# Optimization experiments

Measured on AMD Instinct MI355X. Metric: run time of the kernel, lower is better.

The kernel has to match this reference:

```python
import jax, jax.numpy as jnp
import numpy as np

N, E = 50000, 800000
IN, HID, PROJ = 256, 256, 256


def setup_inputs() -> dict:
    key = jax.random.key(0)
    ks = jax.random.split(key, 6)
    x = jax.random.normal(ks[0], (N, IN), dtype=jnp.float32)
    edge_index = jax.random.randint(ks[1], (2, E), 0, N, dtype=jnp.int32)
    # GCNConv params: Linear (no bias inside lin; bias added after aggregation)
    W1 = jax.random.normal(ks[2], (IN, HID), dtype=jnp.float32) / np.sqrt(IN)
    b1 = jnp.zeros((HID,), dtype=jnp.float32)
    W2 = jax.random.normal(ks[3], (HID, PROJ), dtype=jnp.float32) / np.sqrt(HID)
    b2 = jnp.zeros((PROJ,), dtype=jnp.float32)
    # shared PReLU parameter (PyTorch default init 0.25, single shared scalar)
    a = jnp.asarray(0.25, dtype=jnp.float32)
    return {"x": x, "W1": W1, "b1": b1, "W2": W2, "b2": b2, "a": a,
            "edge_index": edge_index}


def _prelu(x, a):
    return jnp.where(x >= 0, x, a * x)


def _gcn_conv(x, W, b, src, dst, norm):
    # GCNConv: out = D^-1/2 (A + I) D^-1/2 (x W) + b
    h = x @ W                                      # [N, out]
    msg = h[src] * norm[:, None]                   # [E+N, out] edge messages
    out = jax.ops.segment_sum(msg, dst, num_segments=N)
    return out + b


def reference(x, W1, b1, W2, b2, a, edge_index):
    src, dst = edge_index[0], edge_index[1]
    loop = jnp.arange(N, dtype=src.dtype)
    src = jnp.concatenate([src, loop])             # add self-loops
    dst = jnp.concatenate([dst, loop])
    # symmetric normalization (degree counted on dst, as in PyG gcn_norm)
    deg = jax.ops.segment_sum(jnp.ones_like(dst, jnp.float32), dst,
                              num_segments=N)
    dinv = jax.lax.rsqrt(jnp.maximum(deg, 1.0))    # deg >= 1 with self-loops
    norm = dinv[src] * dinv[dst]                   # [E+N]
    h = _prelu(_gcn_conv(x, W1, b1, src, dst, norm), a)
    h = _prelu(_gcn_conv(h, W2, b2, src, dst, norm), a)
    return h
```

## Files before the change

### kernel.cpp

```cpp
#include <hip/hip_runtime.h>

#define NN 50000
#define EE 800000
#define FF 256
#define CAP 64
#define GEMM_BLKS 784
#define FILL_BLKS 3125

typedef float    f32x4 __attribute__((ext_vector_type(4)));
typedef _Float16 f16x8 __attribute__((ext_vector_type(8)));
typedef _Float16 f16x4 __attribute__((ext_vector_type(4)));

__global__ void packw_kernel(const float* __restrict__ W1, const float* __restrict__ W2,
                             _Float16* __restrict__ wp,
                             const int* __restrict__ ei, int* __restrict__ cnt,
                             int* __restrict__ ecw) {
    if (blockIdx.x >= 64) {
        int e = (blockIdx.x - 64) * 256 + threadIdx.x;
        int s = ei[e];
        int d = ei[EE + e];
        int slot = atomicAdd(&cnt[d], 1);
        if (slot < CAP) ecw[(size_t)d * CAP + slot] = s;
        return;
    }
    int idx = blockIdx.x * 256 + threadIdx.x;
    int p   = idx & 511;
    int kt  = (idx >> 9) & 7;
    int nb  = (idx >> 12) & 1;
    int L   = (idx >> 13) & 1;
    const float* W = L ? W2 : W1;
    int rs = p >> 2, cs = p & 3;
    int r  = rs ^ ((rs >> 2) & 1);
    int c  = cs ^ (r & 3);
    int n  = nb * 128 + r;
    int k0 = kt * 32 + c * 8;
    f16x8 hi, lo;
#pragma unroll
    for (int j = 0; j < 8; ++j) {
        float v = W[(size_t)(k0 + j) * 256 + n];
        _Float16 h = (_Float16)v;
        hi[j] = h;
        lo[j] = (_Float16)(v - (float)h);
    }
    size_t ch = ((size_t)((L * 2 + 0) * 2 + nb) * 8 + kt) * 4096;
    size_t cl = ((size_t)((L * 2 + 1) * 2 + nb) * 8 + kt) * 4096;
    *(f16x8*)(wp + ch + (size_t)p * 8) = hi;
    *(f16x8*)(wp + cl + (size_t)p * 8) = lo;
}


__device__ __forceinline__ void gll16(const void* g, void* l) {
    __builtin_amdgcn_global_load_lds(
        (const __attribute__((address_space(1))) void*)g,
        (__attribute__((address_space(3))) void*)l, 16, 0, 0);
}

template<typename AT>
__global__ __launch_bounds__(512) void gemm_kernel(
    const AT* __restrict__ X, const _Float16* __restrict__ Bhi,
    const _Float16* __restrict__ Blo, _Float16* __restrict__ H,
    const int* __restrict__ cnt) {
    __shared__ __align__(16) _Float16 Bh[2][4096];
    __shared__ __align__(16) _Float16 Bl[2][4096];
    __shared__ __align__(16) _Float16 As[2][4096];

    const int gid = blockIdx.x;
    const int p_  = (gid >> 4) * 8 + (gid & 7);
    const int nb  = (gid >> 3) & 1;
    if (p_ >= 391) return;

    const int tid = threadIdx.x;
    const int ln  = tid & 63;
    const int w   = tid >> 6;
    const int wm  = w & 1;
    const int wn  = w >> 1;
    const int q   = ln >> 4;
    const int l16 = ln & 15;
    const int m0  = p_ * 128;
    const size_t bchunk = (size_t)nb * 8 * 4096;

    const int g   = w * 64 + ln;
    const int rs_ = g >> 2, cs_ = g & 3;
    const int r_  = rs_ ^ ((rs_ >> 2) & 1);
    const int c_  = cs_ ^ (r_ & 3);
    int gm_ = m0 + r_; if (gm_ > NN - 1) gm_ = NN - 1;

    f32x4 acc[4][2] = {};

    auto stageB = [&](int kt, int buf) {
        gll16(Bhi + bchunk + (size_t)kt * 4096 + (size_t)g * 8,
              &Bh[buf][w * 512]);
        gll16(Blo + bchunk + (size_t)kt * 4096 + (size_t)g * 8,
              &Bl[buf][w * 512]);
    };
    auto stageA16 = [&](int kt, int buf) {
        gll16((const _Float16*)X + (size_t)gm_ * FF + kt * 32 + c_ * 8,
              (_Float16*)&As[buf][0] + (size_t)(w * 64) * 8);
    };
    auto loadA32 = [&](int kt, f32x4& v0, f32x4& v1) {
        const float* p = (const float*)X + (size_t)gm_ * FF + kt * 32 + c_ * 8;
        v0 = *(const f32x4*)p;
        v1 = *(const f32x4*)(p + 4);
    };
    auto writeA32 = [&](int buf, f32x4 v0, f32x4 v1) {
        f16x8 a;
        a[0] = (_Float16)v0.x; a[1] = (_Float16)v0.y;
        a[2] = (_Float16)v0.z; a[3] = (_Float16)v0.w;
        a[4] = (_Float16)v1.x; a[5] = (_Float16)v1.y;
        a[6] = (_Float16)v1.z; a[7] = (_Float16)v1.w;
        *(f16x8*)(&As[buf][(size_t)g * 8]) = a;
    };

    auto compute = [&](int buf) {
        f16x8 af[4], bhf[2], blf[2];
#pragma unroll
        for (int mt = 0; mt < 4; ++mt) {
            int r  = wm * 64 + mt * 16 + l16;
            int rr = r ^ ((r >> 2) & 1);
            af[mt] = *(const f16x8*)(&As[buf][(rr * 4 + (q ^ (r & 3))) * 8]);
        }
#pragma unroll
        for (int nt = 0; nt < 2; ++nt) {
            int r  = wn * 32 + nt * 16 + l16;
            int rr = r ^ ((r >> 2) & 1);
            int off = (rr * 4 + (q ^ (r & 3))) * 8;
            bhf[nt] = *(const f16x8*)(&Bh[buf][off]);
            blf[nt] = *(const f16x8*)(&Bl[buf][off]);
        }
#pragma unroll
        for (int mt = 0; mt < 4; ++mt)
#pragma unroll
            for (int nt = 0; nt < 2; ++nt) {
                acc[mt][nt] = __builtin_amdgcn_mfma_f32_16x16x32_f16(af[mt], bhf[nt], acc[mt][nt], 0, 0, 0);
                acc[mt][nt] = __builtin_amdgcn_mfma_f32_16x16x32_f16(af[mt], blf[nt], acc[mt][nt], 0, 0, 0);
            }
    };

    int cur = 0;
    if constexpr (sizeof(AT) == 4) {
        f32x4 v0, v1;
        loadA32(0, v0, v1);
        stageB(0, 0);
        writeA32(0, v0, v1);
        __syncthreads();
#pragma unroll
        for (int kt = 0; kt < 8; ++kt) {
            f32x4 n0, n1;
            if (kt < 7) {
                loadA32(kt + 1, n0, n1);
                stageB(kt + 1, cur ^ 1);
            }
            compute(cur);
            if (kt < 7) writeA32(cur ^ 1, n0, n1);
            __syncthreads();
            cur ^= 1;
        }
    } else {
        stageA16(0, 0);
        stageB(0, 0);
        __syncthreads();
#pragma unroll
        for (int kt = 0; kt < 8; ++kt) {
            if (kt < 7) { stageA16(kt + 1, cur ^ 1); stageB(kt + 1, cur ^ 1); }
            compute(cur);
            __syncthreads();
            cur ^= 1;
        }
    }

#pragma unroll
    for (int mt = 0; mt < 4; ++mt)
#pragma unroll
        for (int r4 = 0; r4 < 4; ++r4) {
            int m = m0 + wm * 64 + mt * 16 + q * 4 + r4;
            if (m < NN) {
                float sc = rsqrtf((float)(cnt[m] + 1));
#pragma unroll
                for (int nt = 0; nt < 2; ++nt) {
                    int n = nb * 128 + wn * 32 + nt * 16 + l16;
                    H[(size_t)m * FF + n] = (_Float16)(acc[mt][nt][r4] * sc);
                }
            }
        }
}

template<typename OT>
__global__ __launch_bounds__(256) void agg_kernel(
    const _Float16* __restrict__ H, const int* __restrict__ cnt,
    const int* __restrict__ ecw, const float* __restrict__ bias,
    const float* __restrict__ a_ptr, OT* __restrict__ out) {
    const int row  = blockIdx.x * 4 + (threadIdx.x >> 6);
    const int lane = threadIdx.x & 63;
    if (row >= NN) return;

    const float av  = a_ptr[0];
    const int   deg = cnt[row];
    const float di  = rsqrtf((float)(deg + 1));
    const int   end = (deg < CAP) ? deg : CAP;
    const int*  er  = ecw + (size_t)row * CAP;

    f16x4 hv = *(const f16x4*)(H + (size_t)row * FF + lane * 4);
    float ax = (float)hv.x;
    float ay = (float)hv.y;
    float az = (float)hv.z;
    float aw = (float)hv.w;

    int e = 0;
    for (; e + 7 < end; e += 8) {
        int4 q0 = *(const int4*)(er + e);
        int4 q1 = *(const int4*)(er + e + 4);
        f16x4 h0 = *(const f16x4*)(H + (size_t)q0.x * FF + lane * 4);
        f16x4 h1 = *(const f16x4*)(H + (size_t)q0.y * FF + lane * 4);
        f16x4 h2 = *(const f16x4*)(H + (size_t)q0.z * FF + lane * 4);
        f16x4 h3 = *(const f16x4*)(H + (size_t)q0.w * FF + lane * 4);
        f16x4 h4 = *(const f16x4*)(H + (size_t)q1.x * FF + lane * 4);
        f16x4 h5 = *(const f16x4*)(H + (size_t)q1.y * FF + lane * 4);
        f16x4 h6 = *(const f16x4*)(H + (size_t)q1.z * FF + lane * 4);
        f16x4 h7 = *(const f16x4*)(H + (size_t)q1.w * FF + lane * 4);
        ax += ((float)h0.x + (float)h1.x) + ((float)h2.x + (float)h3.x)
            + ((float)h4.x + (float)h5.x) + ((float)h6.x + (float)h7.x);
        ay += ((float)h0.y + (float)h1.y) + ((float)h2.y + (float)h3.y)
            + ((float)h4.y + (float)h5.y) + ((float)h6.y + (float)h7.y);
        az += ((float)h0.z + (float)h1.z) + ((float)h2.z + (float)h3.z)
            + ((float)h4.z + (float)h5.z) + ((float)h6.z + (float)h7.z);
        aw += ((float)h0.w + (float)h1.w) + ((float)h2.w + (float)h3.w)
            + ((float)h4.w + (float)h5.w) + ((float)h6.w + (float)h7.w);
    }
    for (; e + 3 < end; e += 4) {
        int4 q0 = *(const int4*)(er + e);
        f16x4 h0 = *(const f16x4*)(H + (size_t)q0.x * FF + lane * 4);
        f16x4 h1 = *(const f16x4*)(H + (size_t)q0.y * FF + lane * 4);
        f16x4 h2 = *(const f16x4*)(H + (size_t)q0.z * FF + lane * 4);
        f16x4 h3 = *(const f16x4*)(H + (size_t)q0.w * FF + lane * 4);
        ax += ((float)h0.x + (float)h1.x) + ((float)h2.x + (float)h3.x);
        ay += ((float)h0.y + (float)h1.y) + ((float)h2.y + (float)h3.y);
        az += ((float)h0.z + (float)h1.z) + ((float)h2.z + (float)h3.z);
        aw += ((float)h0.w + (float)h1.w) + ((float)h2.w + (float)h3.w);
    }
    for (; e < end; ++e) {
        int s = er[e];
        f16x4 h0 = *(const f16x4*)(H + (size_t)s * FF + lane * 4);
        ax += (float)h0.x;
        ay += (float)h0.y;
        az += (float)h0.z;
        aw += (float)h0.w;
    }

    f32x4 bv = *(const f32x4*)(bias + lane * 4);
    float r0 = di * ax + bv.x; r0 = (r0 >= 0.f) ? r0 : av * r0;
    float r1 = di * ay + bv.y; r1 = (r1 >= 0.f) ? r1 : av * r1;
    float r2 = di * az + bv.z; r2 = (r2 >= 0.f) ? r2 : av * r2;
    float r3 = di * aw + bv.w; r3 = (r3 >= 0.f) ? r3 : av * r3;
    if constexpr (sizeof(OT) == 4) {
        f32x4 res = {r0, r1, r2, r3};
        *(f32x4*)((float*)out + (size_t)row * FF + lane * 4) = res;
    } else {
        f16x4 res;
        res.x = (_Float16)r0; res.y = (_Float16)r1;
        res.z = (_Float16)r2; res.w = (_Float16)r3;
        *(f16x4*)((_Float16*)out + (size_t)row * FF + lane * 4) = res;
    }
}

extern "C" void kernel_launch(void* const* d_in, const int* in_sizes, int n_in,
                              void* d_out, int out_size, void* d_ws, size_t ws_size,
                              hipStream_t stream) {
    const float* x  = (const float*)d_in[0];
    const float* W1 = (const float*)d_in[1];
    const float* b1 = (const float*)d_in[2];
    const float* W2 = (const float*)d_in[3];
    const float* b2 = (const float*)d_in[4];
    const float* a  = (const float*)d_in[5];
    const int*   ei = (const int*)d_in[6];
    float* out = (float*)d_out;

    char* ws = (char*)d_ws;
    size_t off = 0;
    auto carve = [&](size_t bytes) -> char* {
        char* p = ws + off;
        off = (off + bytes + 255) & ~(size_t)255;
        return p;
    };
    int*      cnt  = (int*)carve((size_t)NN * 4);
    int*      ecw  = (int*)carve((size_t)NN * CAP * 4);
    _Float16* wp   = (_Float16*)carve((size_t)4 * 65536 * 2);
    _Float16* h    = (_Float16*)carve((size_t)NN * FF * 2);
    _Float16* h1   = (_Float16*)carve((size_t)NN * FF * 2);

    hipMemsetAsync(cnt, 0, (size_t)NN * 4, stream);

    packw_kernel<<<64 + FILL_BLKS, 256, 0, stream>>>(W1, W2, wp, ei, cnt, ecw);

    gemm_kernel<float><<<GEMM_BLKS, 512, 0, stream>>>(x, wp, wp + 65536, h, cnt);
    agg_kernel<_Float16><<<(NN + 3) / 4, 256, 0, stream>>>(h, cnt, ecw, b1, a, h1);
    gemm_kernel<_Float16><<<GEMM_BLKS, 512, 0, stream>>>(
        h1, wp + 131072, wp + 131072 + 65536, h, cnt);
    agg_kernel<float><<<(NN + 3) / 4, 256, 0, stream>>>(h, cnt, ecw, b2, a, out);
}
```

Baseline: 317.8 us.

## Pre-convert x to fp16 and deepen GEMM LDS prefetch with manual waitcnts

The fp32→fp16 conversion of x moves into the setup kernel, writing into the h1 buffer, so both GEMM launches share a single fp16 path that loads A directly into LDS. The GEMM main loop now issues loads two k-steps ahead and replaces __syncthreads with explicit vmcnt/lgkmcnt waits, raw s_barrier and sched_barrier fences. This is meant to hide global-load latency better and drop the register round-trip for the A tile. The cost is an extra full pass that reads x and writes an fp16 copy, and the hand-written waitcnt counts are fragile.

```diff
diff --git a/kernel.cpp b/kernel.cpp
--- a/kernel.cpp
+++ b/kernel.cpp
@@ -5,6 +5,7 @@
 #define FF 256
 #define CAP 64
 #define GEMM_BLKS 784
+#define XCVT_BLKS 6250
 #define FILL_BLKS 3125
 
 typedef float    f32x4 __attribute__((ext_vector_type(4)));
@@ -13,17 +14,31 @@
 
 __global__ void packw_kernel(const float* __restrict__ W1, const float* __restrict__ W2,
                              _Float16* __restrict__ wp,
+                             const float* __restrict__ x, _Float16* __restrict__ xh,
                              const int* __restrict__ ei, int* __restrict__ cnt,
                              int* __restrict__ ecw) {
-    if (blockIdx.x >= 64) {
-        int e = (blockIdx.x - 64) * 256 + threadIdx.x;
+    const int bid = blockIdx.x;
+    if (bid >= 64 + XCVT_BLKS) {
+        int e = (bid - 64 - XCVT_BLKS) * 256 + threadIdx.x;
         int s = ei[e];
         int d = ei[EE + e];
         int slot = atomicAdd(&cnt[d], 1);
         if (slot < CAP) ecw[(size_t)d * CAP + slot] = s;
         return;
     }
-    int idx = blockIdx.x * 256 + threadIdx.x;
+    if (bid >= 64) {
+        size_t i = ((size_t)(bid - 64) * 256 + threadIdx.x) * 8;
+        f32x4 v0 = *(const f32x4*)(x + i);
+        f32x4 v1 = *(const f32x4*)(x + i + 4);
+        f16x8 o;
+        o[0] = (_Float16)v0.x; o[1] = (_Float16)v0.y;
+        o[2] = (_Float16)v0.z; o[3] = (_Float16)v0.w;
+        o[4] = (_Float16)v1.x; o[5] = (_Float16)v1.y;
+        o[6] = (_Float16)v1.z; o[7] = (_Float16)v1.w;
+        *(f16x8*)(xh + i) = o;
+        return;
+    }
+    int idx = bid * 256 + threadIdx.x;
     int p   = idx & 511;
     int kt  = (idx >> 9) & 7;
     int nb  = (idx >> 12) & 1;
@@ -55,9 +70,8 @@
         (__attribute__((address_space(3))) void*)l, 16, 0, 0);
 }
 
-template<typename AT>
 __global__ __launch_bounds__(512) void gemm_kernel(
-    const AT* __restrict__ X, const _Float16* __restrict__ Bhi,
+    const _Float16* __restrict__ X, const _Float16* __restrict__ Bhi,
     const _Float16* __restrict__ Blo, _Float16* __restrict__ H,
     const int* __restrict__ cnt) {
     __shared__ __align__(16) _Float16 Bh[2][4096];
@@ -87,28 +101,13 @@
 
     f32x4 acc[4][2] = {};
 
-    auto stageB = [&](int kt, int buf) {
+    auto stage = [&](int kt, int buf) {
         gll16(Bhi + bchunk + (size_t)kt * 4096 + (size_t)g * 8,
               &Bh[buf][w * 512]);
         gll16(Blo + bchunk + (size_t)kt * 4096 + (size_t)g * 8,
               &Bl[buf][w * 512]);
-    };
-    auto stageA16 = [&](int kt, int buf) {
-        gll16((const _Float16*)X + (size_t)gm_ * FF + kt * 32 + c_ * 8,
+        gll16(X + (size_t)gm_ * FF + kt * 32 + c_ * 8,
               (_Float16*)&As[buf][0] + (size_t)(w * 64) * 8);
-    };
-    auto loadA32 = [&](int kt, f32x4& v0, f32x4& v1) {
-        const float* p = (const float*)X + (size_t)gm_ * FF + kt * 32 + c_ * 8;
-        v0 = *(const f32x4*)p;
-        v1 = *(const f32x4*)(p + 4);
-    };
-    auto writeA32 = [&](int buf, f32x4 v0, f32x4 v1) {
-        f16x8 a;
-        a[0] = (_Float16)v0.x; a[1] = (_Float16)v0.y;
-        a[2] = (_Float16)v0.z; a[3] = (_Float16)v0.w;
-        a[4] = (_Float16)v1.x; a[5] = (_Float16)v1.y;
-        a[6] = (_Float16)v1.z; a[7] = (_Float16)v1.w;
-        *(f16x8*)(&As[buf][(size_t)g * 8]) = a;
     };
 
     auto compute = [&](int buf) {
@@ -136,36 +135,23 @@
             }
     };
 
+    stage(0, 0);
+    stage(1, 1);
     int cur = 0;
-    if constexpr (sizeof(AT) == 4) {
-        f32x4 v0, v1;
-        loadA32(0, v0, v1);
-        stageB(0, 0);
-        writeA32(0, v0, v1);
-        __syncthreads();
-#pragma unroll
-        for (int kt = 0; kt < 8; ++kt) {
-            f32x4 n0, n1;
-            if (kt < 7) {
-                loadA32(kt + 1, n0, n1);
-                stageB(kt + 1, cur ^ 1);
-            }
-            compute(cur);
-            if (kt < 7) writeA32(cur ^ 1, n0, n1);
-            __syncthreads();
-            cur ^= 1;
-        }
-    } else {
-        stageA16(0, 0);
-        stageB(0, 0);
-        __syncthreads();
-#pragma unroll
-        for (int kt = 0; kt < 8; ++kt) {
-            if (kt < 7) { stageA16(kt + 1, cur ^ 1); stageB(kt + 1, cur ^ 1); }
-            compute(cur);
-            __syncthreads();
-            cur ^= 1;
-        }
+#pragma unroll
+    for (int kt = 0; kt < 8; ++kt) {
+        if (kt < 7) { asm volatile("s_waitcnt vmcnt(3)" ::: "memory"); }
+        else        { asm volatile("s_waitcnt vmcnt(0)" ::: "memory"); }
+        __builtin_amdgcn_sched_barrier(0);
+        asm volatile("s_barrier" ::: "memory");
+        __builtin_amdgcn_sched_barrier(0);
+        compute(cur);
+        __builtin_amdgcn_sched_barrier(0);
+        asm volatile("s_waitcnt lgkmcnt(0)" ::: "memory");
+        asm volatile("s_barrier" ::: "memory");
+        __builtin_amdgcn_sched_barrier(0);
+        if (kt + 2 < 8) stage(kt + 2, cur);
+        cur ^= 1;
     }
 
 #pragma unroll
@@ -286,14 +272,16 @@
     _Float16* wp   = (_Float16*)carve((size_t)4 * 65536 * 2);
     _Float16* h    = (_Float16*)carve((size_t)NN * FF * 2);
     _Float16* h1   = (_Float16*)carve((size_t)NN * FF * 2);
+    _Float16* xh   = h1;
 
     hipMemsetAsync(cnt, 0, (size_t)NN * 4, stream);
 
-    packw_kernel<<<64 + FILL_BLKS, 256, 0, stream>>>(W1, W2, wp, ei, cnt, ecw);
-
-    gemm_kernel<float><<<GEMM_BLKS, 512, 0, stream>>>(x, wp, wp + 65536, h, cnt);
+    packw_kernel<<<64 + XCVT_BLKS + FILL_BLKS, 256, 0, stream>>>(
+        W1, W2, wp, x, xh, ei, cnt, ecw);
+
+    gemm_kernel<<<GEMM_BLKS, 512, 0, stream>>>(xh, wp, wp + 65536, h, cnt);
     agg_kernel<_Float16><<<(NN + 3) / 4, 256, 0, stream>>>(h, cnt, ecw, b1, a, h1);
-    gemm_kernel<_Float16><<<GEMM_BLKS, 512, 0, stream>>>(
+    gemm_kernel<<<GEMM_BLKS, 512, 0, stream>>>(
         h1, wp + 131072, wp + 131072 + 65536, h, cnt);
     agg_kernel<float><<<(NN + 3) / 4, 256, 0, stream>>>(h, cnt, ecw, b2, a, out);
 }
```

New measurement: 329.2 us. +3.6%, slower.
